# Kernel optimization log

Hardware: AMD Instinct MI355X
Metric: run time of the kernel (lower is better)

## Reference

```python
import jax, jax.numpy as jnp
import numpy as np

BETA = 0.25

def setup_inputs() -> dict:
    key = jax.random.key(0)
    k1, k2 = jax.random.split(key)
    z = jax.random.normal(k1, (4096, 64, 64), dtype=jnp.float32)
    codebooks = jax.random.normal(k2, (64, 256, 64), dtype=jnp.float32)
    return {"z": z, "codebooks": codebooks}

def reference(z, codebooks):
    # z: (B, M, d); codebooks: (M, K, d)
    B, M, d = z.shape
    # squared distances (B, M, K) via ||z||^2 - 2 z.c + ||c||^2 (avoids (B,M,K,d) blowup)
    z2 = jnp.sum(z * z, axis=-1)                      # (B, M)
    c2 = jnp.sum(codebooks * codebooks, axis=-1)      # (M, K)
    zc = jnp.einsum('bmd,mkd->bmk', z, codebooks)     # (B, M, K)
    distances = z2[:, :, None] - 2.0 * zc + c2[None]  # (B, M, K)
    encoding_indices = jnp.argmin(distances, axis=-1) # (B, M) int
    # per-subspace codebook gather: codebooks[m, idx[b, m], :]
    quantized_raw = codebooks[jnp.arange(M)[None, :], encoding_indices]  # (B, M, d)
    # straight-through estimator
    quantized = z + jax.lax.stop_gradient(quantized_raw - z)
    q_loss = (BETA * jnp.mean((jax.lax.stop_gradient(quantized) - z) ** 2)
              + jnp.mean((quantized - jax.lax.stop_gradient(z)) ** 2))
    return quantized, encoding_indices, q_loss
```

## Files before the change

### kernel.cpp

```cpp
#include <hip/hip_runtime.h>

#define IDX_BASE 16777216UL
#define LOSS_IDX 17039360UL
#define EPS2 0.02f

typedef float4 f4;
typedef _Float16 half8 __attribute__((ext_vector_type(8)));
typedef float f32x4 __attribute__((ext_vector_type(4)));

static __device__ __forceinline__ unsigned umax(unsigned a, unsigned b) { return a > b ? a : b; }
static __device__ __forceinline__ unsigned umin(unsigned a, unsigned b) { return a < b ? a : b; }
static __device__ __forceinline__ unsigned f2mono(float s) {
    unsigned u = __float_as_uint(s);
    return u ^ (unsigned)(((int)u >> 31) | 0x80000000);
}
static __device__ __forceinline__ float mono2f(unsigned v) {
    return __uint_as_float(v ^ (((unsigned)((int)(~v) >> 31)) | 0x80000000u));
}

__global__ __launch_bounds__(256) void pq_frag(const float* __restrict__ cb,
                                               half8* __restrict__ fragbuf,
                                               float* __restrict__ c2) {
    int bx = blockIdx.x, tid = threadIdx.x;
    int m = bx >> 2, sub = bx & 3;
    int w = tid >> 6, lane = tid & 63, lh = lane >> 4, l15 = lane & 15;
    const float* cbm = cb + (size_t)m * (256 * 64);
    half8* fbm = fragbuf + (size_t)m * (16 * 4 * 64);
    int tile = w * 4 + sub;
    int code = tile * 16 + l15;
    const float* crow = cbm + code * 64 + lh * 8;
    float ss = 0.f;
    #pragma unroll
    for (int s = 0; s < 2; ++s) {
        f4 a = *reinterpret_cast<const f4*>(crow + s * 32);
        f4 b = *reinterpret_cast<const f4*>(crow + s * 32 + 4);
        float v[8] = {a.x, a.y, a.z, a.w, b.x, b.y, b.z, b.w};
        half8 hi, lo;
        #pragma unroll
        for (int e = 0; e < 8; ++e) {
            _Float16 h = (_Float16)v[e];
            hi[e] = h; lo[e] = (_Float16)(v[e] - (float)h);
            ss = fmaf(v[e], v[e], ss);
        }
        fbm[(tile * 4 + s * 2 + 0) * 64 + lane] = hi;
        fbm[(tile * 4 + s * 2 + 1) * 64 + lane] = lo;
    }
    ss += __shfl_xor(ss, 16, 64);
    ss += __shfl_xor(ss, 32, 64);
    if (lh == 0) c2[m * 256 + code] = ss;
}

__global__ __launch_bounds__(256, 3) void pq_main(
    const float* __restrict__ z, const float* __restrict__ cb,
    const float* __restrict__ c2ws, const half8* __restrict__ fragbuf,
    float* __restrict__ out, float* __restrict__ partial)
{
    __shared__ half8    sZfrag[8 * 4 * 64];
    __shared__ unsigned sK1[4 * 128];
    __shared__ unsigned sK2[4 * 128];
    __shared__ int      sBest[128];
    __shared__ float    sW[4];

    const int tid = threadIdx.x, bx = blockIdx.x;
    const int m = ((bx & 7) << 3) | ((bx >> 3) & 7);
    const int chunk = bx >> 6;
    const int w = tid >> 6, lane = tid & 63;
    const int lh = lane >> 4, l15 = lane & 15;
    const unsigned payBase = 255u - (unsigned)(w * 64 + lh * 4);

    const float* __restrict__ cbm = cb + (size_t)m * (256 * 64);
    const f4* cb4m = reinterpret_cast<const f4*>(cbm);

    #pragma unroll
    for (int i = 0; i < 2; ++i) {
        int rt = w * 2 + i;
        size_t rh = (size_t)(chunk * 128 + rt * 16 + l15);
        const float* zb = z + (rh * 64 + m) * 64 + lh * 8;
        f4 p0 = *reinterpret_cast<const f4*>(zb);
        f4 p1 = *reinterpret_cast<const f4*>(zb + 4);
        f4 p2 = *reinterpret_cast<const f4*>(zb + 32);
        f4 p3 = *reinterpret_cast<const f4*>(zb + 36);
        float v0[8] = {p0.x,p0.y,p0.z,p0.w,p1.x,p1.y,p1.z,p1.w};
        float v1[8] = {p2.x,p2.y,p2.z,p2.w,p3.x,p3.y,p3.z,p3.w};
        half8 h0, l0, h1, l1;
        #pragma unroll
        for (int e = 0; e < 8; ++e) {
            _Float16 a = (_Float16)v0[e];
            h0[e] = a; l0[e] = (_Float16)(v0[e] - (float)a);
            _Float16 b = (_Float16)v1[e];
            h1[e] = b; l1[e] = (_Float16)(v1[e] - (float)b);
        }
        sZfrag[rt * 256 +   0 + lane] = h0;
        sZfrag[rt * 256 +  64 + lane] = l0;
        sZfrag[rt * 256 + 128 + lane] = h1;
        sZfrag[rt * 256 + 192 + lane] = l1;
    }

    const half8* __restrict__ fb = fragbuf + (size_t)m * (16 * 4 * 64);
    half8 ah[4][2], al[4][2];
    #pragma unroll
    for (int t = 0; t < 4; ++t) {
        #pragma unroll
        for (int s = 0; s < 2; ++s) {
            ah[t][s] = fb[((w * 4 + t) * 4 + s * 2 + 0) * 64 + lane];
            al[t][s] = fb[((w * 4 + t) * 4 + s * 2 + 1) * 64 + lane];
        }
    }
    const f4* __restrict__ c2t = reinterpret_cast<const f4*>(c2ws + m * 256);
    f32x4 c2i[4];
    #pragma unroll
    for (int t = 0; t < 4; ++t) {
        f4 cv = c2t[(w * 4 + t) * 4 + lh];
        c2i[t][0] = -0.5f*cv.x; c2i[t][1] = -0.5f*cv.y;
        c2i[t][2] = -0.5f*cv.z; c2i[t][3] = -0.5f*cv.w;
    }

    __syncthreads();

    #pragma unroll 1
    for (int rt = 0; rt < 8; ++rt) {
        const half8* zf = &sZfrag[rt * 256 + lane];
        half8 bh0 = zf[0], bl0 = zf[64], bh1 = zf[128], bl1 = zf[192];
        unsigned K1 = 0u, K2 = 0u;
        #pragma unroll
        for (int t = 0; t < 4; ++t) {
            const unsigned pb = payBase - (unsigned)(t * 16);
            f32x4 acc = c2i[t];
            acc = __builtin_amdgcn_mfma_f32_16x16x32_f16(ah[t][0], bh0, acc, 0, 0, 0);
            acc = __builtin_amdgcn_mfma_f32_16x16x32_f16(ah[t][1], bh1, acc, 0, 0, 0);
            acc = __builtin_amdgcn_mfma_f32_16x16x32_f16(ah[t][0], bl0, acc, 0, 0, 0);
            acc = __builtin_amdgcn_mfma_f32_16x16x32_f16(ah[t][1], bl1, acc, 0, 0, 0);
            acc = __builtin_amdgcn_mfma_f32_16x16x32_f16(al[t][0], bh0, acc, 0, 0, 0);
            acc = __builtin_amdgcn_mfma_f32_16x16x32_f16(al[t][1], bh1, acc, 0, 0, 0);
            unsigned kk0 = (f2mono(acc[0]) & 0xFFFFFF00u) | (pb - 0u);
            unsigned kk1 = (f2mono(acc[1]) & 0xFFFFFF00u) | (pb - 1u);
            unsigned kk2 = (f2mono(acc[2]) & 0xFFFFFF00u) | (pb - 2u);
            unsigned kk3 = (f2mono(acc[3]) & 0xFFFFFF00u) | (pb - 3u);
            unsigned a  = umax(kk0, kk1), b2 = umin(kk0, kk1);
            unsigned c  = umax(kk2, kk3), d  = umin(kk2, kk3);
            unsigned t1 = umax(a, c);
            unsigned t2 = umax(umin(a, c), umax(b2, d));
            K2 = umax(umax(K2, t2), umin(K1, t1));
            K1 = umax(K1, t1);
        }
        #pragma unroll
        for (int off = 16; off <= 32; off <<= 1) {
            unsigned o1 = (unsigned)__shfl_xor((int)K1, off, 64);
            unsigned o2 = (unsigned)__shfl_xor((int)K2, off, 64);
            K2 = umax(umax(K2, o2), umin(K1, o1));
            K1 = umax(K1, o1);
        }
        if (lane < 16) {
            sK1[w * 128 + rt * 16 + lane] = K1;
            sK2[w * 128 + rt * 16 + lane] = K2;
        }
    }
    __syncthreads();

    if (tid < 128) {
        unsigned G1 = 0u, G2 = 0u;
        #pragma unroll
        for (int w2 = 0; w2 < 4; ++w2) {
            unsigned k1w = sK1[w2 * 128 + tid];
            unsigned k2w = sK2[w2 * 128 + tid];
            G2 = umax(umax(G2, k2w), umin(G1, k1w));
            G1 = umax(G1, k1w);
        }
        float s1 = mono2f(G1 & 0xFFFFFF00u);
        float s2 = mono2f(G2 & 0xFFFFFF00u);
        sBest[tid] = (s1 - s2 < EPS2) ? -1 : (int)(255u - (G1 & 0xFFu));
    }
    __syncthreads();

    for (int row = w; row < 128; row += 4) {
        if (sBest[row] >= 0) continue;
        size_t rg = (size_t)(chunk * 128 + row);
        const f4* zr4 = reinterpret_cast<const f4*>(z + (rg * 64 + m) * 64);
        float bs = -1e30f; int bk = 0;
        #pragma unroll 1
        for (int j = 0; j < 4; ++j) {
            int k = j * 64 + lane;
            float s = -0.5f * c2ws[m * 256 + k];
            #pragma unroll
            for (int d4 = 0; d4 < 16; ++d4) {
                f4 cvv = cb4m[k * 16 + d4];
                f4 zz  = zr4[d4];
                s = fmaf(zz.x, cvv.x, s); s = fmaf(zz.y, cvv.y, s);
                s = fmaf(zz.z, cvv.z, s); s = fmaf(zz.w, cvv.w, s);
            }
            if (s > bs) { bs = s; bk = k; }
        }
        #pragma unroll
        for (int off = 1; off < 64; off <<= 1) {
            float ov = __shfl_xor(bs, off, 64);
            int   ok = __shfl_xor(bk, off, 64);
            if (ov > bs || (ov == bs && ok < bk)) { bs = ov; bk = ok; }
        }
        if (lane == 0) sBest[row] = bk;
    }
    __syncthreads();

    float lsum = 0.f;
    {
        int row = tid >> 1, hf = tid & 1;
        int k = sBest[row];
        size_t b = (size_t)(chunk * 128 + row);
        const f4* q4 = cb4m + (size_t)k * 16 + hf * 8;
        const f4* z4 = reinterpret_cast<const f4*>(z + (b * 64 + m) * 64) + hf * 8;
        f4*       o4 = reinterpret_cast<f4*>(out + (b * 64 + m) * 64) + hf * 8;
        float l0 = 0.f, l1 = 0.f;
        #pragma unroll
        for (int c = 0; c < 8; ++c) {
            f4 qv = q4[c], zv = z4[c];
            o4[c] = qv;
            float d0 = qv.x - zv.x, d1 = qv.y - zv.y, d2 = qv.z - zv.z, d3 = qv.w - zv.w;
            l0 = fmaf(d0, d0, l0); l1 = fmaf(d1, d1, l1);
            l0 = fmaf(d2, d2, l0); l1 = fmaf(d3, d3, l1);
        }
        lsum = l0 + l1;
    }
    if (tid < 128)
        out[IDX_BASE + (size_t)(chunk * 128 + tid) * 64 + m] = (float)sBest[tid];
    #pragma unroll
    for (int off = 1; off < 64; off <<= 1) lsum += __shfl_xor(lsum, off, 64);
    if (lane == 0) sW[w] = lsum;
    __syncthreads();
    if (tid == 0) partial[bx] = (sW[0] + sW[1]) + (sW[2] + sW[3]);
}

__global__ __launch_bounds__(256) void pq_loss(const float* __restrict__ partial,
                                               float* __restrict__ out)
{
    __shared__ float sW[4];
    float s = 0.f;
    #pragma unroll
    for (int i = 0; i < 8; ++i) s += partial[threadIdx.x + i * 256];
    #pragma unroll
    for (int off = 1; off < 64; off <<= 1) s += __shfl_xor(s, off, 64);
    if ((threadIdx.x & 63) == 0) sW[threadIdx.x >> 6] = s;
    __syncthreads();
    if (threadIdx.x == 0)
        out[LOSS_IDX] = ((sW[0] + sW[1]) + (sW[2] + sW[3])) * (1.25f / 16777216.0f);
}

extern "C" void kernel_launch(void* const* d_in, const int* in_sizes, int n_in,
                              void* d_out, int out_size, void* d_ws, size_t ws_size,
                              hipStream_t stream) {
    const float* zp  = (const float*)d_in[0];
    const float* cbp = (const float*)d_in[1];
    float* outp = (float*)d_out;
    float* c2ws = (float*)d_ws;
    half8* frag = (half8*)((float*)d_ws + 16384);
    float* part = (float*)d_ws + 16384 + 1048576;

    pq_frag<<<dim3(256),  dim3(256), 0, stream>>>(cbp, frag, c2ws);
    pq_main<<<dim3(2048), dim3(256), 0, stream>>>(zp, cbp, c2ws, frag, outp, part);
    pq_loss<<<dim3(1),    dim3(256), 0, stream>>>(part, outp);
}
```

Baseline: 94.01 us.

## Use 512-thread blocks splitting codes across 8 waves, reuse LDS z in epilogue

```diff
diff --git a/kernel.cpp b/kernel.cpp
--- a/kernel.cpp
+++ b/kernel.cpp
@@ -50,31 +50,29 @@
     if (lh == 0) c2[m * 256 + code] = ss;
 }
 
-__global__ __launch_bounds__(256, 3) void pq_main(
+__global__ __launch_bounds__(512, 4) void pq_main(
     const float* __restrict__ z, const float* __restrict__ cb,
     const float* __restrict__ c2ws, const half8* __restrict__ fragbuf,
     float* __restrict__ out, float* __restrict__ partial)
 {
     __shared__ half8    sZfrag[8 * 4 * 64];
-    __shared__ unsigned sK1[4 * 128];
-    __shared__ unsigned sK2[4 * 128];
+    __shared__ unsigned sK1[8 * 128];
+    __shared__ unsigned sK2[8 * 128];
     __shared__ int      sBest[128];
-    __shared__ float    sW[4];
+    __shared__ float    sW[8];
 
     const int tid = threadIdx.x, bx = blockIdx.x;
     const int m = ((bx & 7) << 3) | ((bx >> 3) & 7);
     const int chunk = bx >> 6;
     const int w = tid >> 6, lane = tid & 63;
     const int lh = lane >> 4, l15 = lane & 15;
-    const unsigned payBase = 255u - (unsigned)(w * 64 + lh * 4);
+    const unsigned payBase = 255u - (unsigned)(w * 32 + lh * 4);
 
     const float* __restrict__ cbm = cb + (size_t)m * (256 * 64);
     const f4* cb4m = reinterpret_cast<const f4*>(cbm);
 
-    #pragma unroll
-    for (int i = 0; i < 2; ++i) {
-        int rt = w * 2 + i;
-        size_t rh = (size_t)(chunk * 128 + rt * 16 + l15);
+    {
+        size_t rh = (size_t)(chunk * 128 + w * 16 + l15);
         const float* zb = z + (rh * 64 + m) * 64 + lh * 8;
         f4 p0 = *reinterpret_cast<const f4*>(zb);
         f4 p1 = *reinterpret_cast<const f4*>(zb + 4);
@@ -90,27 +88,27 @@
             _Float16 b = (_Float16)v1[e];
             h1[e] = b; l1[e] = (_Float16)(v1[e] - (float)b);
         }
-        sZfrag[rt * 256 +   0 + lane] = h0;
-        sZfrag[rt * 256 +  64 + lane] = l0;
-        sZfrag[rt * 256 + 128 + lane] = h1;
-        sZfrag[rt * 256 + 192 + lane] = l1;
+        sZfrag[w * 256 +   0 + lane] = h0;
+        sZfrag[w * 256 +  64 + lane] = l0;
+        sZfrag[w * 256 + 128 + lane] = h1;
+        sZfrag[w * 256 + 192 + lane] = l1;
     }
 
     const half8* __restrict__ fb = fragbuf + (size_t)m * (16 * 4 * 64);
-    half8 ah[4][2], al[4][2];
-    #pragma unroll
-    for (int t = 0; t < 4; ++t) {
+    half8 ah[2][2], al[2][2];
+    #pragma unroll
+    for (int t = 0; t < 2; ++t) {
         #pragma unroll
         for (int s = 0; s < 2; ++s) {
-            ah[t][s] = fb[((w * 4 + t) * 4 + s * 2 + 0) * 64 + lane];
-            al[t][s] = fb[((w * 4 + t) * 4 + s * 2 + 1) * 64 + lane];
+            ah[t][s] = fb[((w * 2 + t) * 4 + s * 2 + 0) * 64 + lane];
+            al[t][s] = fb[((w * 2 + t) * 4 + s * 2 + 1) * 64 + lane];
         }
     }
     const f4* __restrict__ c2t = reinterpret_cast<const f4*>(c2ws + m * 256);
-    f32x4 c2i[4];
-    #pragma unroll
-    for (int t = 0; t < 4; ++t) {
-        f4 cv = c2t[(w * 4 + t) * 4 + lh];
+    f32x4 c2i[2];
+    #pragma unroll
+    for (int t = 0; t < 2; ++t) {
+        f4 cv = c2t[(w * 2 + t) * 4 + lh];
         c2i[t][0] = -0.5f*cv.x; c2i[t][1] = -0.5f*cv.y;
         c2i[t][2] = -0.5f*cv.z; c2i[t][3] = -0.5f*cv.w;
     }
@@ -123,7 +121,7 @@
         half8 bh0 = zf[0], bl0 = zf[64], bh1 = zf[128], bl1 = zf[192];
         unsigned K1 = 0u, K2 = 0u;
         #pragma unroll
-        for (int t = 0; t < 4; ++t) {
+        for (int t = 0; t < 2; ++t) {
             const unsigned pb = payBase - (unsigned)(t * 16);
             f32x4 acc = c2i[t];
             acc = __builtin_amdgcn_mfma_f32_16x16x32_f16(ah[t][0], bh0, acc, 0, 0, 0);
@@ -160,7 +158,7 @@
     if (tid < 128) {
         unsigned G1 = 0u, G2 = 0u;
         #pragma unroll
-        for (int w2 = 0; w2 < 4; ++w2) {
+        for (int w2 = 0; w2 < 8; ++w2) {
             unsigned k1w = sK1[w2 * 128 + tid];
             unsigned k2w = sK2[w2 * 128 + tid];
             G2 = umax(umax(G2, k2w), umin(G1, k1w));
@@ -172,7 +170,7 @@
     }
     __syncthreads();
 
-    for (int row = w; row < 128; row += 4) {
+    for (int row = w; row < 128; row += 8) {
         if (sBest[row] >= 0) continue;
         size_t rg = (size_t)(chunk * 128 + row);
         const f4* zr4 = reinterpret_cast<const f4*>(z + (rg * 64 + m) * 64);
@@ -202,22 +200,38 @@
 
     float lsum = 0.f;
     {
-        int row = tid >> 1, hf = tid & 1;
+        int row = tid >> 2, q = tid & 3;
         int k = sBest[row];
+        int rt2 = row >> 4, rr = row & 15;
+        int uh = (q >= 2) ? 2 : 0;
+        int lh0 = (q & 1) * 2;
+        half8 hi0 = sZfrag[(rt2 * 4 + uh)     * 64 + lh0 * 16 + 16 + rr - 16];
+        half8 hi1 = sZfrag[(rt2 * 4 + uh)     * 64 + (lh0 + 1) * 16 + rr];
+        half8 lo0 = sZfrag[(rt2 * 4 + uh + 1) * 64 + lh0 * 16 + rr];
+        half8 lo1 = sZfrag[(rt2 * 4 + uh + 1) * 64 + (lh0 + 1) * 16 + rr];
         size_t b = (size_t)(chunk * 128 + row);
-        const f4* q4 = cb4m + (size_t)k * 16 + hf * 8;
-        const f4* z4 = reinterpret_cast<const f4*>(z + (b * 64 + m) * 64) + hf * 8;
-        f4*       o4 = reinterpret_cast<f4*>(out + (b * 64 + m) * 64) + hf * 8;
-        float l0 = 0.f, l1 = 0.f;
-        #pragma unroll
-        for (int c = 0; c < 8; ++c) {
-            f4 qv = q4[c], zv = z4[c];
-            o4[c] = qv;
-            float d0 = qv.x - zv.x, d1 = qv.y - zv.y, d2 = qv.z - zv.z, d3 = qv.w - zv.w;
-            l0 = fmaf(d0, d0, l0); l1 = fmaf(d1, d1, l1);
-            l0 = fmaf(d2, d2, l0); l1 = fmaf(d3, d3, l1);
-        }
-        lsum = l0 + l1;
+        const f4* q4 = cb4m + (size_t)k * 16 + q * 4;
+        f4*       o4 = reinterpret_cast<f4*>(out + (b * 64 + m) * 64) + q * 4;
+        float l0s = 0.f, l1s = 0.f;
+        #pragma unroll
+        for (int c = 0; c < 2; ++c) {
+            f4 qa = q4[c * 2], qb = q4[c * 2 + 1];
+            const half8& hh = c ? hi1 : hi0;
+            const half8& ll = c ? lo1 : lo0;
+            float zr0 = (float)hh[0] + (float)ll[0], zr1 = (float)hh[1] + (float)ll[1];
+            float zr2 = (float)hh[2] + (float)ll[2], zr3 = (float)hh[3] + (float)ll[3];
+            float zr4 = (float)hh[4] + (float)ll[4], zr5 = (float)hh[5] + (float)ll[5];
+            float zr6 = (float)hh[6] + (float)ll[6], zr7 = (float)hh[7] + (float)ll[7];
+            o4[c * 2]     = qa;
+            o4[c * 2 + 1] = qb;
+            float d0 = qa.x - zr0, d1 = qa.y - zr1, d2 = qa.z - zr2, d3 = qa.w - zr3;
+            float d4 = qb.x - zr4, d5 = qb.y - zr5, d6 = qb.z - zr6, d7 = qb.w - zr7;
+            l0s = fmaf(d0, d0, l0s); l1s = fmaf(d1, d1, l1s);
+            l0s = fmaf(d2, d2, l0s); l1s = fmaf(d3, d3, l1s);
+            l0s = fmaf(d4, d4, l0s); l1s = fmaf(d5, d5, l1s);
+            l0s = fmaf(d6, d6, l0s); l1s = fmaf(d7, d7, l1s);
+        }
+        lsum = l0s + l1s;
     }
     if (tid < 128)
         out[IDX_BASE + (size_t)(chunk * 128 + tid) * 64 + m] = (float)sBest[tid];
@@ -225,7 +239,12 @@
     for (int off = 1; off < 64; off <<= 1) lsum += __shfl_xor(lsum, off, 64);
     if (lane == 0) sW[w] = lsum;
     __syncthreads();
-    if (tid == 0) partial[bx] = (sW[0] + sW[1]) + (sW[2] + sW[3]);
+    if (tid == 0) {
+        float t = 0.f;
+        #pragma unroll
+        for (int i = 0; i < 8; ++i) t += sW[i];
+        partial[bx] = t;
+    }
 }
 
 __global__ __launch_bounds__(256) void pq_loss(const float* __restrict__ partial,
@@ -254,6 +273,6 @@
     float* part = (float*)d_ws + 16384 + 1048576;
 
     pq_frag<<<dim3(256),  dim3(256), 0, stream>>>(cbp, frag, c2ws);
-    pq_main<<<dim3(2048), dim3(256), 0, stream>>>(zp, cbp, c2ws, frag, outp, part);
+    pq_main<<<dim3(2048), dim3(512), 0, stream>>>(zp, cbp, c2ws, frag, outp, part);
     pq_loss<<<dim3(1),    dim3(256), 0, stream>>>(part, outp);
 }
```

Measured after the change: 82.53 us. -12.2%, faster.
